# Optimization experiments

Hardware: AMD Instinct MI355X
Metric: run time of the kernel (lower is better)

## Reference

```python
import jax, jax.numpy as jnp
import numpy as np

N, G, P = 512, 11560, 2000
E_SG, E_GP, E_PP = 1000000, 200000, 50000
HID, HEADS, L = 192, 4, 2
C = HID // HEADS
NQ, OUT = 20, 128
EPS = 1e-5


def setup_inputs():
    key = jax.random.key(0)
    ks = iter(jax.random.split(key, 64))
    def rn(shape, s=0.05):
        return jax.random.normal(next(ks), shape, jnp.float32) * s
    def ri(n, hi):
        return jax.random.randint(next(ks), (n,), 0, hi)
    return dict(
        x_sample=rn((N, HID), 1.0), x_gene=rn((G, HID), 1.0), x_pathway=rn((P, HID), 1.0),
        e_sg_src=ri(E_SG, N), e_sg_dst=ri(E_SG, G),
        e_gp_src=ri(E_GP, G), e_gp_dst=ri(E_GP, P),
        e_pp_src=ri(E_PP, P), e_pp_dst=ri(E_PP, P),
        sage_Wl=rn((L, 2, HID, HID)), sage_bl=jnp.zeros((L, 2, HID)), sage_Wr=rn((L, 2, HID, HID)),
        gat_Wl=rn((L, 3, HID, HID)), gat_bl=jnp.zeros((L, 3, HID)),
        gat_Wr=rn((L, 3, HID, HID)), gat_br=jnp.zeros((L, 3, HID)),
        gat_att=rn((L, 3, HEADS, C), 0.1), gat_bias=jnp.zeros((L, 3, HID)),
        ln_g=jnp.ones((L, 3, HID)), ln_b=jnp.zeros((L, 3, HID)),
        pool_query=rn((NQ, HID), 1.0),
        pool_in_w=rn((3 * HID, HID)), pool_in_b=jnp.zeros((3 * HID,)),
        pool_out_w=rn((HID, HID)), pool_out_b=jnp.zeros((HID,)),
        ff_w1=rn((HID, HID)), ff_b1=jnp.zeros((HID,)),
        ff_w2=rn((HID, HID)), ff_b2=jnp.zeros((HID,)),
        pool_ln_g=jnp.ones((HID,)), pool_ln_b=jnp.zeros((HID,)),
        proj_w=rn((OUT, HID)), proj_b=jnp.zeros((OUT,)),
    )


def _ln(x, g, b):
    mu = x.mean(-1, keepdims=True)
    v = ((x - mu) ** 2).mean(-1, keepdims=True)
    return (x - mu) / jnp.sqrt(v + EPS) * g + b


def _sage(x_src, x_dst, src, dst, Wl, bl, Wr, n_dst):
    # PyG SAGEConv: lin_l(mean_aggr(x_src[neighbors])) + lin_r(x_dst)
    s = jax.ops.segment_sum(x_src[src], dst, num_segments=n_dst)
    cnt = jax.ops.segment_sum(jnp.ones((src.shape[0],), x_src.dtype), dst, num_segments=n_dst)
    mean = s / jnp.maximum(cnt, 1.0)[:, None]
    return mean @ Wl.T + bl + x_dst @ Wr.T


def _gatv2(x_src, x_dst, src, dst, Wl, bl, Wr, br, att, bias, n_dst):
    # transform nodes first (cheap), then gather per edge
    gl = (x_src @ Wl.T + bl).reshape(-1, HEADS, C)[src]   # [E,H,C]
    gr = (x_dst @ Wr.T + br).reshape(-1, HEADS, C)[dst]   # [E,H,C]
    e = jax.nn.leaky_relu(gl + gr, 0.2)
    score = jnp.einsum('ehc,hc->eh', e, att)              # [E,H]
    m = jax.ops.segment_max(score, dst, num_segments=n_dst)
    ex = jnp.exp(score - m[dst])
    den = jax.ops.segment_sum(ex, dst, num_segments=n_dst)
    alpha = ex / (den[dst] + 1e-16)
    out = jax.ops.segment_sum(alpha[:, :, None] * gl, dst, num_segments=n_dst)
    return out.reshape(n_dst, HID) + bias


def reference(x_sample, x_gene, x_pathway, e_sg_src, e_sg_dst, e_gp_src, e_gp_dst,
              e_pp_src, e_pp_dst, sage_Wl, sage_bl, sage_Wr, gat_Wl, gat_bl, gat_Wr,
              gat_br, gat_att, gat_bias, ln_g, ln_b, pool_query, pool_in_w, pool_in_b,
              pool_out_w, pool_out_b, ff_w1, ff_b1, ff_w2, ff_b2, pool_ln_g, pool_ln_b,
              proj_w, proj_b):
    xs, xg, xp = x_sample, x_gene, x_pathway
    for l in range(L):
        og = _sage(xs, xg, e_sg_src, e_sg_dst, sage_Wl[l, 0], sage_bl[l, 0], sage_Wr[l, 0], G)
        os_ = _sage(xg, xs, e_sg_dst, e_sg_src, sage_Wl[l, 1], sage_bl[l, 1], sage_Wr[l, 1], N)
        op = _gatv2(xg, xp, e_gp_src, e_gp_dst, gat_Wl[l, 0], gat_bl[l, 0], gat_Wr[l, 0],
                    gat_br[l, 0], gat_att[l, 0], gat_bias[l, 0], P)
        og = og + _gatv2(xp, xg, e_gp_dst, e_gp_src, gat_Wl[l, 1], gat_bl[l, 1], gat_Wr[l, 1],
                         gat_br[l, 1], gat_att[l, 1], gat_bias[l, 1], G)
        op = op + _gatv2(xp, xp, e_pp_src, e_pp_dst, gat_Wl[l, 2], gat_bl[l, 2], gat_Wr[l, 2],
                         gat_br[l, 2], gat_att[l, 2], gat_bias[l, 2], P)
        # residual + LayerNorm (dropout = identity in eval)
        xs = _ln(xs + os_, ln_g[l, 0], ln_b[l, 0])
        xg = _ln(xg + og, ln_g[l, 1], ln_b[l, 1])
        xp = _ln(xp + op, ln_g[l, 2], ln_b[l, 2])
    # MultiQueryPooling over sample nodes (batch=1 MultiheadAttention)
    Wq, Wk, Wv = jnp.split(pool_in_w, 3, axis=0)
    bq, bk, bv = jnp.split(pool_in_b, 3, axis=0)
    q = (pool_query @ Wq.T + bq).reshape(NQ, HEADS, C)
    k = (xs @ Wk.T + bk).reshape(N, HEADS, C)
    v = (xs @ Wv.T + bv).reshape(N, HEADS, C)
    attn = jax.nn.softmax(jnp.einsum('qhc,nhc->hqn', q, k) / (C ** 0.5), axis=-1)
    o = jnp.einsum('hqn,nhc->qhc', attn, v).reshape(NQ, HID) @ pool_out_w.T + pool_out_b
    pooled = o.mean(0)  # [HID]
    h = jax.nn.relu(pooled @ ff_w1.T + ff_b1) @ ff_w2.T + ff_b2
    h = _ln(h, pool_ln_g, pool_ln_b)
    return (h @ proj_w.T + proj_b)[None, :]  # [1, OUT]
```

## Files before the change

kernel.cpp:

```cpp
#include <hip/hip_runtime.h>

#define N_S 512
#define N_G 11560
#define N_P 2000
#define NE_SG 1000000
#define NE_GP 200000
#define NE_PP 50000
#define HID 192
#define HEADS 4
#define CDIM 48
#define NQd 20
#define OUTD 128
#define LDK 12288
#define SPLITK 16
#define CHUNKK 768

typedef __attribute__((ext_vector_type(8))) short short8;
typedef __attribute__((ext_vector_type(4))) float float4v;

__device__ __forceinline__ float bf2f(unsigned short u){
  union { unsigned int i; float f; } x; x.i = ((unsigned int)u) << 16; return x.f;
}
__device__ __forceinline__ unsigned short f2bf(float f){
  union { float f; unsigned int i; } u; u.f = f;
  unsigned int r = u.i + 0x7FFFu + ((u.i >> 16) & 1u);
  return (unsigned short)(r >> 16);
}
__device__ __forceinline__ ushort4 f4bf(float4 v){
  return make_ushort4(f2bf(v.x), f2bf(v.y), f2bf(v.z), f2bf(v.w));
}

__global__ __launch_bounds__(256) void k_detect(const unsigned int* __restrict__ raw,
                                                int* __restrict__ flag){
  __shared__ int cnt;
  if (threadIdx.x == 0) cnt = 0;
  __syncthreads();
  int c = 0;
  for (int i = threadIdx.x; i < 2048; i += 256) {
    float f = __uint_as_float(raw[i]);
    float a = fabsf(f);
    if (f == f && a > 1e-4f && a < 1000.0f) c++;
  }
  atomicAdd(&cnt, c);
  __syncthreads();
  if (threadIdx.x == 0) flag[0] = (cnt >= 1024) ? 1 : 0;
}

#define NLOAD 27
#define LOADBX 2048
struct LoadDesc { const void* src; float* dst; int n; };
struct LoadTable { LoadDesc d[NLOAD]; };
__global__ __launch_bounds__(256)
void k_load_all(LoadTable tab, const int* __restrict__ flag){
  LoadDesc de = tab.d[blockIdx.y];
  int fp32 = flag[0];
  for (int i = blockIdx.x*256 + threadIdx.x; i < de.n; i += LOADBX*256) {
    if (fp32) de.dst[i] = ((const float*)de.src)[i];
    else      de.dst[i] = bf2f(((const unsigned short*)de.src)[i]);
  }
}

__global__ __launch_bounds__(256)
void k_cntbuild(const int* __restrict__ src, const int* __restrict__ dst,
                int* __restrict__ cg, int E){
  int i = blockIdx.x*256 + threadIdx.x;
  if (i >= E) return;
  atomicAdd(&cg[(size_t)dst[i]*N_S + src[i]], 1);
}

__global__ __launch_bounds__(256)
void k_cvtT(const int* __restrict__ cg, unsigned short* __restrict__ bfA,
            unsigned short* __restrict__ bfB){
  __shared__ unsigned short tile[64][68];
  int g0 = blockIdx.x*64, s0 = blockIdx.y*64;
  int t = threadIdx.x; int r = t>>2, seg = t&3;
  int g = g0 + r;
  if (g < N_G) {
    const int* row = cg + (size_t)g*N_S + s0 + seg*16;
    unsigned short* arow = bfA + (size_t)g*N_S + s0 + seg*16;
    #pragma unroll
    for (int i=0;i<16;i++){
      unsigned short v = f2bf((float)row[i]);
      tile[r][seg*16+i] = v;
      arow[i] = v;
    }
  } else {
    #pragma unroll
    for (int i=0;i<16;i++) tile[r][seg*16+i] = 0;
  }
  __syncthreads();
  int s = s0 + r;
  unsigned short* brow = bfB + (size_t)s*LDK + g0 + seg*16;
  #pragma unroll
  for (int i=0;i<16;i++) brow[i] = tile[seg*16+i][r];
}

__global__ __launch_bounds__(256)
void k_rowinv_i(const int* __restrict__ A, int lda, int cols, int n,
                float* __restrict__ outp){
  int row = blockIdx.x*4 + (threadIdx.x >> 6);
  if (row >= n) return;
  int lane = threadIdx.x & 63;
  const int* Ar = A + (size_t)row*lda;
  float s = 0.0f;
  for (int c = lane; c < cols; c += 64) s += (float)Ar[c];
  #pragma unroll
  for (int o = 32; o; o >>= 1) s += __shfl_xor(s, o);
  if (lane == 0) outp[row] = 1.0f / fmaxf(s, 1.0f);
}
__global__ __launch_bounds__(256)
void k_rowinv_h(const unsigned short* __restrict__ A, int lda, int cols, int n,
                float* __restrict__ outp){
  int row = blockIdx.x*4 + (threadIdx.x >> 6);
  if (row >= n) return;
  int lane = threadIdx.x & 63;
  const unsigned short* Ar = A + (size_t)row*lda;
  float s = 0.0f;
  for (int c = lane; c < cols; c += 64) s += bf2f(Ar[c]);
  #pragma unroll
  for (int o = 32; o; o >>= 1) s += __shfl_xor(s, o);
  if (lane == 0) outp[row] = 1.0f / fmaxf(s, 1.0f);
}

__global__ __launch_bounds__(256)
void k_transpose(const float* __restrict__ in, unsigned short* __restrict__ outp,
                 int n, int ldo){
  __shared__ float tile[64][65];
  int r0 = blockIdx.x*64, c0 = blockIdx.y*64;
  int t = threadIdx.x;
  int r = t >> 2, seg = t & 3;
  int grr = r0 + r;
  if (grr < n) {
    #pragma unroll
    for (int i = 0; i < 4; i++) {
      float4 v = *(const float4*)(in + (size_t)grr*HID + c0 + seg*16 + i*4);
      tile[r][seg*16+i*4+0] = v.x; tile[r][seg*16+i*4+1] = v.y;
      tile[r][seg*16+i*4+2] = v.z; tile[r][seg*16+i*4+3] = v.w;
    }
  } else {
    #pragma unroll
    for (int i = 0; i < 16; i++) tile[r][seg*16+i] = 0.0f;
  }
  __syncthreads();
  int w = t >> 6, lane = t & 63;
  if (r0 + lane < ldo) {
    #pragma unroll
    for (int j = 0; j < 16; j++) {
      int c = w*16 + j;
      outp[(size_t)(c0+c)*ldo + r0 + lane] = f2bf(tile[lane][c]);
    }
  }
}

struct CsrJob { const int* src; const int* dst; int E; int n;
                int* deg; int* rowptr; int* cursor; int* col; };
struct CsrJobs { CsrJob j[3]; };

__global__ __launch_bounds__(256) void k_hist3(CsrJobs jobs){
  CsrJob jb = jobs.j[blockIdx.y];
  int i = blockIdx.x*256 + threadIdx.x;
  if (i < jb.E) atomicAdd(&jb.deg[jb.dst[i]], 1);
}
__global__ __launch_bounds__(256) void k_scan3(CsrJobs jobs){
  CsrJob jb = jobs.j[blockIdx.x];
  __shared__ int part[256];
  __shared__ int pre[256];
  int t = threadIdx.x;
  int n = jb.n;
  int C = (n + 255) >> 8;
  int lo = t*C, hi = min(n, lo + C);
  int s = 0;
  for (int i = lo; i < hi; i++) s += jb.deg[i];
  part[t] = s;
  __syncthreads();
  if (t == 0) {
    int acc = 0;
    for (int i = 0; i < 256; i++) { pre[i] = acc; acc += part[i]; }
    jb.rowptr[n] = acc;
  }
  __syncthreads();
  int run = pre[t];
  for (int i = lo; i < hi; i++) {
    jb.rowptr[i] = run; jb.cursor[i] = run; run += jb.deg[i];
  }
}
__global__ __launch_bounds__(256) void k_fill3(CsrJobs jobs){
  CsrJob jb = jobs.j[blockIdx.y];
  int i = blockIdx.x*256 + threadIdx.x;
  if (i >= jb.E) return;
  int pos = atomicAdd(&jb.cursor[jb.dst[i]], 1);
  jb.col[pos] = jb.src[i];
}

#define LDA 200
__global__ __launch_bounds__(256)
void k_gemm(const float* __restrict__ A, const float* __restrict__ rowscale,
            const float* __restrict__ W, const float* __restrict__ bias,
            float* __restrict__ outp, int n, int accum)
{
  __shared__ __align__(16) unsigned short Asm[64*LDA];
  __shared__ __align__(16) unsigned short Wsm[64*LDA];
  int t = threadIdx.x;
  int row0 = blockIdx.x * 64;
  int col0 = blockIdx.y * 64;
  {
    int r = t >> 2, seg = t & 3;
    int gr = row0 + r;
    unsigned short* ad = Asm + r*LDA + seg*48;
    if (gr < n) {
      float sc = rowscale ? rowscale[gr] : 1.0f;
      const float* Ar = A + (size_t)gr*HID + seg*48;
      #pragma unroll
      for (int i = 0; i < 12; i++) {
        float4 v = *reinterpret_cast<const float4*>(Ar + i*4);
        v.x *= sc; v.y *= sc; v.z *= sc; v.w *= sc;
        *reinterpret_cast<ushort4*>(ad + i*4) = f4bf(v);
      }
    } else {
      ushort4 z = make_ushort4(0,0,0,0);
      #pragma unroll
      for (int i = 0; i < 12; i++) *reinterpret_cast<ushort4*>(ad + i*4) = z;
    }
    const float* Wr = W + (size_t)(col0 + r)*HID + seg*48;
    unsigned short* wd = Wsm + r*LDA + seg*48;
    #pragma unroll
    for (int i = 0; i < 12; i++) {
      float4 v = *reinterpret_cast<const float4*>(Wr + i*4);
      *reinterpret_cast<ushort4*>(wd + i*4) = f4bf(v);
    }
  }
  __syncthreads();
  int w = t >> 6, lane = t & 63;
  int quad = lane >> 4, mr = lane & 15;
  float4v acc[4] = {};
  const unsigned short* Abase = Asm + (w*16 + mr)*LDA + quad*8;
  const unsigned short* Wbase = Wsm + mr*LDA + quad*8;
  #pragma unroll
  for (int k0 = 0; k0 < 6; k0++) {
    short8 a = *reinterpret_cast<const short8*>(Abase + k0*32);
    #pragma unroll
    for (int ct = 0; ct < 4; ct++) {
      short8 b = *reinterpret_cast<const short8*>(Wbase + ct*16*LDA + k0*32);
      acc[ct] = __builtin_amdgcn_mfma_f32_16x16x32_bf16(a, b, acc[ct], 0, 0, 0);
    }
  }
  #pragma unroll
  for (int ct = 0; ct < 4; ct++) {
    #pragma unroll
    for (int reg = 0; reg < 4; reg++) {
      int rr = row0 + w*16 + quad*4 + reg;
      if (rr < n) {
        int cc = col0 + ct*16 + mr;
        float v = acc[ct][reg];
        if (bias) v += bias[cc];
        if (accum) v += outp[(size_t)rr*HID + cc];
        outp[(size_t)rr*HID + cc] = v;
      }
    }
  }
}

struct GemmJob { const float* A; const float* W; const float* bias;
                 unsigned short* out; int n; };
struct GemmJobs { GemmJob j[6]; int rb[7]; };
__global__ __launch_bounds__(256)
void k_gemm6(GemmJobs jobs)
{
  int bx = blockIdx.x;
  int z = 0;
  #pragma unroll
  for (int q = 1; q < 6; q++) if (bx >= jobs.rb[q]) z = q;
  GemmJob jb = jobs.j[z];
  int row0 = (bx - jobs.rb[z]) * 64;
  __shared__ __align__(16) unsigned short Asm[64*LDA];
  __shared__ __align__(16) unsigned short Wsm[64*LDA];
  int t = threadIdx.x;
  int col0 = blockIdx.y * 64;
  {
    int r = t >> 2, seg = t & 3;
    int gr = row0 + r;
    unsigned short* ad = Asm + r*LDA + seg*48;
    if (gr < jb.n) {
      const float* Ar = jb.A + (size_t)gr*HID + seg*48;
      #pragma unroll
      for (int i = 0; i < 12; i++) {
        float4 v = *reinterpret_cast<const float4*>(Ar + i*4);
        *reinterpret_cast<ushort4*>(ad + i*4) = f4bf(v);
      }
    } else {
      ushort4 zz = make_ushort4(0,0,0,0);
      #pragma unroll
      for (int i = 0; i < 12; i++) *reinterpret_cast<ushort4*>(ad + i*4) = zz;
    }
    const float* Wr = jb.W + (size_t)(col0 + r)*HID + seg*48;
    unsigned short* wd = Wsm + r*LDA + seg*48;
    #pragma unroll
    for (int i = 0; i < 12; i++) {
      float4 v = *reinterpret_cast<const float4*>(Wr + i*4);
      *reinterpret_cast<ushort4*>(wd + i*4) = f4bf(v);
    }
  }
  __syncthreads();
  int w = t >> 6, lane = t & 63;
  int quad = lane >> 4, mr = lane & 15;
  float4v acc[4] = {};
  const unsigned short* Abase = Asm + (w*16 + mr)*LDA + quad*8;
  const unsigned short* Wbase = Wsm + mr*LDA + quad*8;
  #pragma unroll
  for (int k0 = 0; k0 < 6; k0++) {
    short8 a = *reinterpret_cast<const short8*>(Abase + k0*32);
    #pragma unroll
    for (int ct = 0; ct < 4; ct++) {
      short8 b = *reinterpret_cast<const short8*>(Wbase + ct*16*LDA + k0*32);
      acc[ct] = __builtin_amdgcn_mfma_f32_16x16x32_bf16(a, b, acc[ct], 0, 0, 0);
    }
  }
  #pragma unroll
  for (int ct = 0; ct < 4; ct++) {
    #pragma unroll
    for (int reg = 0; reg < 4; reg++) {
      int rr = row0 + w*16 + quad*4 + reg;
      if (rr < jb.n) {
        int cc = col0 + ct*16 + mr;
        jb.out[(size_t)rr*HID + cc] = f2bf(acc[ct][reg] + jb.bias[cc]);
      }
    }
  }
}

__global__ __launch_bounds__(256)
void k_gemm2(const float* __restrict__ A1, const float* __restrict__ rs1,
             const float* __restrict__ W1,
             const float* __restrict__ A2, const float* __restrict__ W2,
             const float* __restrict__ bias,
             float* __restrict__ outp, int n)
{
  __shared__ __align__(16) unsigned short Asm[64*LDA];
  __shared__ __align__(16) unsigned short Wsm[64*LDA];
  int t = threadIdx.x;
  int row0 = blockIdx.x * 64;
  int col0 = blockIdx.y * 64;
  int r = t >> 2, seg = t & 3;
  int w = t >> 6, lane = t & 63;
  int quad = lane >> 4, mr = lane & 15;
  float4v acc[4] = {};
  for (int p = 0; p < 2; p++) {
    if (p) __syncthreads();
    const float* A = p ? A2 : A1;
    const float* W = p ? W2 : W1;
    {
      int gr = row0 + r;
      unsigned short* ad = Asm + r*LDA + seg*48;
      if (gr < n) {
        float sc = (!p && rs1) ? rs1[gr] : 1.0f;
        const float* Ar = A + (size_t)gr*HID + seg*48;
        #pragma unroll
        for (int i = 0; i < 12; i++) {
          float4 v = *reinterpret_cast<const float4*>(Ar + i*4);
          v.x *= sc; v.y *= sc; v.z *= sc; v.w *= sc;
          *reinterpret_cast<ushort4*>(ad + i*4) = f4bf(v);
        }
      } else {
        ushort4 z = make_ushort4(0,0,0,0);
        #pragma unroll
        for (int i = 0; i < 12; i++) *reinterpret_cast<ushort4*>(ad + i*4) = z;
      }
      const float* Wr = W + (size_t)(col0 + r)*HID + seg*48;
      unsigned short* wd = Wsm + r*LDA + seg*48;
      #pragma unroll
      for (int i = 0; i < 12; i++) {
        float4 v = *reinterpret_cast<const float4*>(Wr + i*4);
        *reinterpret_cast<ushort4*>(wd + i*4) = f4bf(v);
      }
    }
    __syncthreads();
    const unsigned short* Abase = Asm + (w*16 + mr)*LDA + quad*8;
    const unsigned short* Wbase = Wsm + mr*LDA + quad*8;
    #pragma unroll
    for (int k0 = 0; k0 < 6; k0++) {
      short8 a = *reinterpret_cast<const short8*>(Abase + k0*32);
      #pragma unroll
      for (int ct = 0; ct < 4; ct++) {
        short8 b = *reinterpret_cast<const short8*>(Wbase + ct*16*LDA + k0*32);
        acc[ct] = __builtin_amdgcn_mfma_f32_16x16x32_bf16(a, b, acc[ct], 0, 0, 0);
      }
    }
  }
  #pragma unroll
  for (int ct = 0; ct < 4; ct++) {
    #pragma unroll
    for (int reg = 0; reg < 4; reg++) {
      int rr = row0 + w*16 + quad*4 + reg;
      if (rr < n) {
        int cc = col0 + ct*16 + mr;
        outp[(size_t)rr*HID + cc] = acc[ct][reg] + bias[cc];
      }
    }
  }
}

#define BKG 128
#define LDG 136
__global__ __launch_bounds__(256)
void k_gemm_g(const unsigned short* __restrict__ A, int lda,
              const unsigned short* __restrict__ W, int ldw,
              float* __restrict__ outp, int n, int K)
{
  __shared__ __align__(16) unsigned short Asm[64*LDG];
  __shared__ __align__(16) unsigned short Wsm[64*LDG];
  int t = threadIdx.x;
  int row0 = blockIdx.x * 64;
  int col0 = blockIdx.y * 64;
  int r = t >> 2, seg = t & 3;
  int w = t >> 6, lane = t & 63;
  int quad = lane >> 4, mr = lane & 15;
  float4v acc[4] = {};
  for (int k0 = 0; k0 < K; k0 += BKG) {
    {
      int gr = row0 + r;
      unsigned short* ad = Asm + r*LDG + seg*32;
      if (gr < n) {
        const unsigned short* Ar = A + (size_t)gr*lda + k0 + seg*32;
        #pragma unroll
        for (int i = 0; i < 4; i++) *(uint4*)(ad + i*8) = *(const uint4*)(Ar + i*8);
      } else {
        uint4 z = make_uint4(0,0,0,0);
        #pragma unroll
        for (int i = 0; i < 4; i++) *(uint4*)(ad + i*8) = z;
      }
      const unsigned short* Wr = W + (size_t)(col0 + r)*ldw + k0 + seg*32;
      unsigned short* wd = Wsm + r*LDG + seg*32;
      #pragma unroll
      for (int i = 0; i < 4; i++) *(uint4*)(wd + i*8) = *(const uint4*)(Wr + i*8);
    }
    __syncthreads();
    const unsigned short* Abase = Asm + (w*16 + mr)*LDG + quad*8;
    const unsigned short* Wbase = Wsm + mr*LDG + quad*8;
    #pragma unroll
    for (int kk = 0; kk < 4; kk++) {
      short8 a = *(const short8*)(Abase + kk*32);
      #pragma unroll
      for (int ct = 0; ct < 4; ct++) {
        short8 b = *(const short8*)(Wbase + ct*16*LDG + kk*32);
        acc[ct] = __builtin_amdgcn_mfma_f32_16x16x32_bf16(a, b, acc[ct], 0, 0, 0);
      }
    }
    __syncthreads();
  }
  #pragma unroll
  for (int ct = 0; ct < 4; ct++) {
    #pragma unroll
    for (int reg = 0; reg < 4; reg++) {
      int rr = row0 + w*16 + quad*4 + reg;
      if (rr < n) outp[(size_t)rr*HID + col0 + ct*16 + mr] = acc[ct][reg];
    }
  }
}

__global__ __launch_bounds__(256)
void k_gemm_sk(const unsigned short* __restrict__ A, int lda,
               const unsigned short* __restrict__ W, int ldw,
               float* __restrict__ part, int n)
{
  __shared__ __align__(16) unsigned short Asm[64*LDG];
  __shared__ __align__(16) unsigned short Wsm[64*LDG];
  int t = threadIdx.x;
  int row0 = blockIdx.x * 64;
  int col0 = blockIdx.y * 64;
  int kz   = blockIdx.z;
  int kbeg = kz * CHUNKK;
  int r = t >> 2, seg = t & 3;
  int w = t >> 6, lane = t & 63;
  int quad = lane >> 4, mr = lane & 15;
  float4v acc[4] = {};
  for (int k0 = kbeg; k0 < kbeg + CHUNKK; k0 += BKG) {
    {
      int gr = row0 + r;
      unsigned short* ad = Asm + r*LDG + seg*32;
      if (gr < n) {
        const unsigned short* Ar = A + (size_t)gr*lda + k0 + seg*32;
        #pragma unroll
        for (int i = 0; i < 4; i++) *(uint4*)(ad + i*8) = *(const uint4*)(Ar + i*8);
      } else {
        uint4 z = make_uint4(0,0,0,0);
        #pragma unroll
        for (int i = 0; i < 4; i++) *(uint4*)(ad + i*8) = z;
      }
      const unsigned short* Wr = W + (size_t)(col0 + r)*ldw + k0 + seg*32;
      unsigned short* wd = Wsm + r*LDG + seg*32;
      #pragma unroll
      for (int i = 0; i < 4; i++) *(uint4*)(wd + i*8) = *(const uint4*)(Wr + i*8);
    }
    __syncthreads();
    const unsigned short* Abase = Asm + (w*16 + mr)*LDG + quad*8;
    const unsigned short* Wbase = Wsm + mr*LDG + quad*8;
    #pragma unroll
    for (int kk = 0; kk < 4; kk++) {
      short8 a = *(const short8*)(Abase + kk*32);
      #pragma unroll
      for (int ct = 0; ct < 4; ct++) {
        short8 b = *(const short8*)(Wbase + ct*16*LDG + kk*32);
        acc[ct] = __builtin_amdgcn_mfma_f32_16x16x32_bf16(a, b, acc[ct], 0, 0, 0);
      }
    }
    __syncthreads();
  }
  float* pd = part + (size_t)kz*n*HID;
  #pragma unroll
  for (int ct = 0; ct < 4; ct++) {
    #pragma unroll
    for (int reg = 0; reg < 4; reg++) {
      int rr = row0 + w*16 + quad*4 + reg;
      if (rr < n) pd[(size_t)rr*HID + col0 + ct*16 + mr] = acc[ct][reg];
    }
  }
}

__global__ __launch_bounds__(256)
void k_reduce_sk(const float* __restrict__ part, float* __restrict__ outp, int n){
  int i = blockIdx.x*256 + threadIdx.x;
  if (i >= n*HID) return;
  float s = 0.0f;
  #pragma unroll
  for (int z = 0; z < SPLITK; z++) s += part[(size_t)z*n*HID + i];
  outp[i] = s;
}

struct GatJob { const unsigned short* gl; const unsigned short* gr;
                const int* rowptr; const int* col;
                const float* att; const float* bias; float* out; int ndst; int accum; };
struct GatJobs { GatJob j[3]; int bo[4]; };

__global__ __launch_bounds__(256)
void k_gat_all(GatJobs jobs)
{
  int bx = blockIdx.x;
  int jz = 0;
  if (bx >= jobs.bo[1]) jz = 1;
  if (bx >= jobs.bo[2]) jz = 2;
  GatJob jb = jobs.j[jz];
  int tid = threadIdx.x;
  int w = tid >> 6, lane = tid & 63;
  int dst = (bx - jobs.bo[jz])*4 + w;
  bool active = dst < jb.ndst;
  __shared__ float attS[HID];
  __shared__ float grS[4][HID];
  __shared__ float swS[4][4][16];
  __shared__ int   sidxS[4][16];
  __shared__ float fS[4][4];
  __shared__ float lS[4][4];
  if (tid < HID) attS[tid] = jb.att[tid];
  if (active) {
    const unsigned short* grr = jb.gr + (size_t)dst*HID;
    grS[w][lane]     = bf2f(grr[lane]);
    grS[w][lane+64]  = bf2f(grr[lane+64]);
    grS[w][lane+128] = bf2f(grr[lane+128]);
  }
  __syncthreads();
  if (!active) return;

  int h16 = lane >> 4, j16 = lane & 15;
  int start = jb.rowptr[dst], end = jb.rowptr[dst+1];
  float m = -1e30f, l = 0.0f;
  float acc0 = 0.f, acc1 = 0.f, acc2 = 0.f;
  int hd0 = lane/48, hd1 = (lane+64)/48, hd2 = (lane+128)/48;
  const float* attH = attS + h16*CDIM;
  const float* grH  = grS[w] + h16*CDIM;

  for (int c0 = start; c0 < end; c0 += 16) {
    int nc = min(16, end - c0);
    float sc = -1e30f; int s = -1;
    if (j16 < nc) {
      s = jb.col[c0 + j16];
      const unsigned short* glr = jb.gl + (size_t)s*HID + h16*CDIM;
      float a = 0.0f;
      #pragma unroll
      for (int c = 0; c < CDIM; c++) {
        float v = bf2f(glr[c]) + grH[c];
        v = v > 0.0f ? v : 0.2f*v;
        a += v * attH[c];
      }
      sc = a;
    }
    if (h16 == 0) sidxS[w][j16] = s;
    float cm = sc;
    cm = fmaxf(cm, __shfl_xor(cm, 1));
    cm = fmaxf(cm, __shfl_xor(cm, 2));
    cm = fmaxf(cm, __shfl_xor(cm, 4));
    cm = fmaxf(cm, __shfl_xor(cm, 8));
    float nm = fmaxf(m, cm);
    float f = __expf(m - nm);
    l *= f;
    float e = (j16 < nc) ? __expf(sc - nm) : 0.0f;
    swS[w][h16][j16] = e;
    float cl = e;
    cl += __shfl_xor(cl, 1);
    cl += __shfl_xor(cl, 2);
    cl += __shfl_xor(cl, 4);
    cl += __shfl_xor(cl, 8);
    l += cl;
    m = nm;
    if (j16 == 0) fS[w][h16] = f;
    acc0 *= fS[w][hd0]; acc1 *= fS[w][hd1]; acc2 *= fS[w][hd2];
    for (int j = 0; j < nc; j++) {
      const unsigned short* glr = jb.gl + (size_t)sidxS[w][j]*HID;
      acc0 += swS[w][hd0][j] * bf2f(glr[lane]);
      acc1 += swS[w][hd1][j] * bf2f(glr[lane+64]);
      acc2 += swS[w][hd2][j] * bf2f(glr[lane+128]);
    }
  }
  if (j16 == 0) lS[w][h16] = l;
  float* od = jb.out + (size_t)dst*HID;
  float v0 = acc0 / (lS[w][hd0] + 1e-16f) + jb.bias[lane];
  float v1 = acc1 / (lS[w][hd1] + 1e-16f) + jb.bias[lane+64];
  float v2 = acc2 / (lS[w][hd2] + 1e-16f) + jb.bias[lane+128];
  if (jb.accum) { v0 += od[lane]; v1 += od[lane+64]; v2 += od[lane+128]; }
  od[lane] = v0; od[lane+64] = v1; od[lane+128] = v2;
}

__global__ __launch_bounds__(64)
void k_ln3(float* __restrict__ xs, const float* __restrict__ osb,
           float* __restrict__ xg, const float* __restrict__ og,
           float* __restrict__ xp, const float* __restrict__ opb,
           const float* __restrict__ op2,
           const float* __restrict__ LNg, const float* __restrict__ LNb, int l)
{
  int r = blockIdx.x;
  float* x; const float* d1; const float* d2 = nullptr; int typ;
  if (r < N_S)            { x = xs + (size_t)r*HID; d1 = osb + (size_t)r*HID; typ = 0; }
  else if (r < N_S + N_G) { int rr = r - N_S; x = xg + (size_t)rr*HID; d1 = og + (size_t)rr*HID; typ = 1; }
  else                    { int rr = r - N_S - N_G; x = xp + (size_t)rr*HID; d1 = opb + (size_t)rr*HID;
                            d2 = op2 + (size_t)rr*HID; typ = 2; }
  const float* g = LNg + (l*3 + typ)*HID;
  const float* b = LNb + (l*3 + typ)*HID;
  int lane = threadIdx.x;
  float v[3]; float sum = 0.0f;
  #pragma unroll
  for (int j=0;j<3;j++){
    int d = j*64 + lane;
    float t = x[d] + d1[d];
    if (d2) t += d2[d];
    v[j] = t; sum += t;
  }
  #pragma unroll
  for (int o=32;o;o>>=1) sum += __shfl_xor(sum, o);
  float mu = sum * (1.0f/HID);
  float var = 0.0f;
  #pragma unroll
  for (int j=0;j<3;j++){ float dd = v[j]-mu; var += dd*dd; }
  #pragma unroll
  for (int o=32;o;o>>=1) var += __shfl_xor(var, o);
  var *= (1.0f/HID);
  float inv = rsqrtf(var + 1e-5f);
  #pragma unroll
  for (int j=0;j<3;j++){
    int d = j*64 + lane;
    x[d] = (v[j]-mu)*inv*g[d] + b[d];
  }
}

__global__ __launch_bounds__(256)
void k_pool_attn(const float* __restrict__ qb, const float* __restrict__ kb,
                 const float* __restrict__ vb, float* __restrict__ ob)
{
  int h = blockIdx.x & 3;
  int q = blockIdx.x >> 2;
  __shared__ float prob[N_S];
  __shared__ float red[256];
  int t = threadIdx.x;
  const float* qrow = qb + (size_t)q*HID + h*CDIM;
  const float scale = 0.14433756729740643f;
  for (int n = t; n < N_S; n += 256) {
    const float* krow = kb + (size_t)n*HID + h*CDIM;
    float s = 0.0f;
    #pragma unroll 8
    for (int c=0;c<CDIM;c++) s += qrow[c]*krow[c];
    prob[n] = s * scale;
  }
  __syncthreads();
  float m = -1e30f;
  for (int n=t;n<N_S;n+=256) m = fmaxf(m, prob[n]);
  red[t] = m; __syncthreads();
  for (int s2=128;s2;s2>>=1){ if (t<s2) red[t]=fmaxf(red[t],red[t+s2]); __syncthreads(); }
  m = red[0]; __syncthreads();
  float sum = 0.0f;
  for (int n=t;n<N_S;n+=256){ float e=__expf(prob[n]-m); prob[n]=e; sum+=e; }
  red[t] = sum; __syncthreads();
  for (int s2=128;s2;s2>>=1){ if (t<s2) red[t]+=red[t+s2]; __syncthreads(); }
  float inv = 1.0f/red[0];
  __syncthreads();
  if (t < CDIM) {
    float acc = 0.0f;
    for (int n=0;n<N_S;n++) acc += prob[n]*vb[(size_t)n*HID + h*CDIM + t];
    ob[(size_t)q*HID + h*CDIM + t] = acc * inv;
  }
}

__global__ __launch_bounds__(192)
void k_tail(const float* __restrict__ ob2,
            const float* ffw1, const float* ffb1,
            const float* ffw2, const float* ffb2,
            const float* lng, const float* lnb,
            const float* pw, const float* pb,
            void* __restrict__ outp, const int* __restrict__ flag)
{
  __shared__ float pooled[HID];
  __shared__ float hh[HID];
  __shared__ float stats[2];
  int t = threadIdx.x;
  float a = 0.0f;
  for (int q=0;q<NQd;q++) a += ob2[q*HID + t];
  pooled[t] = a * (1.0f/NQd);
  __syncthreads();
  float s1 = ffb1[t];
  for (int k=0;k<HID;k++) s1 += pooled[k]*ffw1[t*HID+k];
  hh[t] = fmaxf(s1, 0.0f);
  __syncthreads();
  float s2 = ffb2[t];
  for (int k=0;k<HID;k++) s2 += hh[k]*ffw2[t*HID+k];
  __syncthreads();
  hh[t] = s2;
  __syncthreads();
  if (t == 0) {
    float mu=0.0f; for (int k=0;k<HID;k++) mu += hh[k];
    mu *= (1.0f/HID);
    float v=0.0f; for (int k=0;k<HID;k++){ float d=hh[k]-mu; v+=d*d; }
    v *= (1.0f/HID);
    stats[0]=mu; stats[1]=rsqrtf(v + 1e-5f);
  }
  __syncthreads();
  pooled[t] = (hh[t]-stats[0])*stats[1]*lng[t] + lnb[t];
  __syncthreads();
  if (t < OUTD) {
    float acc = pb[t];
    for (int k=0;k<HID;k++) acc += pooled[k]*pw[t*HID+k];
    if (flag[0]) ((float*)outp)[t] = acc;
    else         ((unsigned short*)outp)[t] = f2bf(acc);
  }
}

extern "C" void kernel_launch(void* const* d_in, const int* in_sizes, int n_in,
                              void* d_out, int out_size, void* d_ws, size_t ws_size,
                              hipStream_t stream)
{
  const int* sg_src = (const int*)d_in[3];
  const int* sg_dst = (const int*)d_in[4];
  const int* gp_src = (const int*)d_in[5];
  const int* gp_dst = (const int*)d_in[6];
  const int* pp_src = (const int*)d_in[7];
  const int* pp_dst = (const int*)d_in[8];

  float* base = (float*)d_ws;
  size_t off = 0;
  auto alloc = [&](size_t nf){ nf = (nf + 3) & ~(size_t)3; float* p = base + off; off += nf; return p; };
  int*   flag = (int*)alloc(4);
  float* xs   = alloc((size_t)N_S*HID);
  float* xg   = alloc((size_t)N_G*HID);
  float* xp   = alloc((size_t)N_P*HID);
  float* qin  = alloc((size_t)NQd*HID);
  float* Wsl  = alloc(2*2*HID*HID); float* bsl = alloc(2*2*HID); float* Wsr = alloc(2*2*HID*HID);
  float* Wgl  = alloc(2*3*HID*HID); float* bgl = alloc(2*3*HID);
  float* Wgr  = alloc(2*3*HID*HID); float* bgr = alloc(2*3*HID);
  float* Agat = alloc(2*3*HEADS*CDIM); float* Bgat = alloc(2*3*HID);
  float* LNg  = alloc(2*3*HID); float* LNb = alloc(2*3*HID);
  float* Pinw = alloc(3*HID*HID); float* Pinb = alloc(3*HID);
  float* Poutw= alloc(HID*HID);   float* Poutb= alloc(HID);
  float* Fw1  = alloc(HID*HID);   float* Fb1  = alloc(HID);
  float* Fw2  = alloc(HID*HID);   float* Fb2  = alloc(HID);
  float* PLg  = alloc(HID);       float* PLb  = alloc(HID);
  float* Pw   = alloc(OUTD*HID);  float* Pb   = alloc(OUTD);
  float* agg  = alloc((size_t)N_G*HID);
  float* aggS = alloc((size_t)N_S*HID);
  float* og   = alloc((size_t)N_G*HID);
  float* osb  = alloc((size_t)N_S*HID);
  float* opb  = alloc((size_t)N_P*HID);
  float* op2  = alloc((size_t)N_P*HID);
  unsigned short* glGb  = (unsigned short*)alloc((size_t)N_G*HID/2);
  unsigned short* grGb  = (unsigned short*)alloc((size_t)N_G*HID/2);
  unsigned short* grP0b = (unsigned short*)alloc((size_t)N_P*HID/2);
  unsigned short* glP1b = (unsigned short*)alloc((size_t)N_P*HID/2);
  unsigned short* glP2b = (unsigned short*)alloc((size_t)N_P*HID/2);
  unsigned short* grP2b = (unsigned short*)alloc((size_t)N_P*HID/2);
  float* qbuf = alloc((size_t)NQd*HID);
  float* kbuf = alloc((size_t)N_S*HID);
  float* vbuf = alloc((size_t)N_S*HID);
  float* obuf = alloc((size_t)NQd*HID);
  float* ob2  = alloc((size_t)NQd*HID);
  int*            CntGi = (int*)alloc((size_t)N_G*N_S);
  unsigned short* CntGb = (unsigned short*)alloc((size_t)N_G*N_S/2);
  unsigned short* CntSb = (unsigned short*)alloc((size_t)N_S*LDK/2);
  unsigned short* xsTb  = (unsigned short*)alloc((size_t)HID*N_S/2);
  unsigned short* xgTb  = (unsigned short*)alloc((size_t)HID*LDK/2);
  float* part = alloc((size_t)SPLITK*N_S*HID);
  float* invdegG = alloc(N_G);
  float* invdegS = alloc(N_S);
  int* degAll = (int*)alloc(2*N_P + N_G + 4);
  int* curAll = (int*)alloc(2*N_P + N_G + 4);
  int* rp_gp_p = (int*)alloc(N_P+2);  int* col_gp_p = (int*)alloc(NE_GP);
  int* rp_gp_g = (int*)alloc(N_G+2);  int* col_gp_g = (int*)alloc(NE_GP);
  int* rp_pp_p = (int*)alloc(N_P+2);  int* col_pp_p = (int*)alloc(NE_PP);
  (void)ws_size; (void)in_sizes; (void)n_in; (void)out_size;

  k_detect<<<1,256,0,stream>>>((const unsigned int*)d_in[0], flag);

  {
    LoadTable tab;
    int k = 0;
    auto add = [&](int i, float* dst, int n){ tab.d[k].src = d_in[i]; tab.d[k].dst = dst; tab.d[k].n = n; k++; };
    add(0,  xs,  N_S*HID);  add(1,  xg,  N_G*HID);  add(2,  xp,  N_P*HID);
    add(9,  Wsl, 2*2*HID*HID); add(10, bsl, 2*2*HID); add(11, Wsr, 2*2*HID*HID);
    add(12, Wgl, 2*3*HID*HID); add(13, bgl, 2*3*HID);
    add(14, Wgr, 2*3*HID*HID); add(15, bgr, 2*3*HID);
    add(16, Agat, 2*3*HEADS*CDIM); add(17, Bgat, 2*3*HID);
    add(18, LNg, 2*3*HID); add(19, LNb, 2*3*HID);
    add(20, qin, NQd*HID);
    add(21, Pinw, 3*HID*HID); add(22, Pinb, 3*HID);
    add(23, Poutw, HID*HID);  add(24, Poutb, HID);
    add(25, Fw1, HID*HID); add(26, Fb1, HID);
    add(27, Fw2, HID*HID); add(28, Fb2, HID);
    add(29, PLg, HID); add(30, PLb, HID);
    add(31, Pw, OUTD*HID); add(32, Pb, OUTD);
    k_load_all<<<dim3(LOADBX, NLOAD),256,0,stream>>>(tab, flag);
  }

  hipMemsetAsync(CntGi, 0, (size_t)N_G*N_S*4, stream);
  hipMemsetAsync(degAll, 0, (size_t)(2*N_P + N_G)*4, stream);
  k_cntbuild<<<(NE_SG+255)/256,256,0,stream>>>(sg_src, sg_dst, CntGi, NE_SG);
  k_cvtT<<<dim3(LDK/64, N_S/64),256,0,stream>>>(CntGi, CntGb, CntSb);
  k_rowinv_i<<<(N_G+3)/4,256,0,stream>>>(CntGi, N_S, N_S, N_G, invdegG);
  k_rowinv_h<<<(N_S+3)/4,256,0,stream>>>(CntSb, LDK, LDK, N_S, invdegS);

  {
    CsrJobs jobs;
    jobs.j[0] = { gp_src, gp_dst, NE_GP, N_P, degAll,           rp_gp_p, curAll,           col_gp_p };
    jobs.j[1] = { gp_dst, gp_src, NE_GP, N_G, degAll+N_P,       rp_gp_g, curAll+N_P,       col_gp_g };
    jobs.j[2] = { pp_src, pp_dst, NE_PP, N_P, degAll+N_P+N_G,   rp_pp_p, curAll+N_P+N_G,   col_pp_p };
    k_hist3<<<dim3((NE_GP+255)/256, 3),256,0,stream>>>(jobs);
    k_scan3<<<3,256,0,stream>>>(jobs);
    k_fill3<<<dim3((NE_GP+255)/256, 3),256,0,stream>>>(jobs);
  }

  const int RB_G = (N_G+63)/64, RB_P = (N_P+63)/64;
  const int GB_P = (N_P+3)/4,  GB_G = (N_G+3)/4;

  for (int l=0; l<2; l++) {
    k_transpose<<<dim3(8,3),256,0,stream>>>(xs, xsTb, N_S, N_S);
    k_gemm_g<<<dim3(RB_G,3),256,0,stream>>>(CntGb, N_S, xsTb, N_S, agg, N_G, N_S);
    k_gemm2<<<dim3(RB_G,3),256,0,stream>>>(agg, invdegG,
        Wsl + (size_t)(l*2+0)*HID*HID, xg, Wsr + (size_t)(l*2+0)*HID*HID,
        bsl + (l*2+0)*HID, og, N_G);

    k_transpose<<<dim3(LDK/64,3),256,0,stream>>>(xg, xgTb, N_G, LDK);
    k_gemm_sk<<<dim3(8,3,SPLITK),256,0,stream>>>(CntSb, LDK, xgTb, LDK, part, N_S);
    k_reduce_sk<<<(N_S*HID+255)/256,256,0,stream>>>(part, aggS, N_S);
    k_gemm2<<<dim3((N_S+63)/64,3),256,0,stream>>>(aggS, invdegS,
        Wsl + (size_t)(l*2+1)*HID*HID, xs, Wsr + (size_t)(l*2+1)*HID*HID,
        bsl + (l*2+1)*HID, osb, N_S);

    {
      GemmJobs gj;
      int w0 = l*3+0, w1 = l*3+1, w2 = l*3+2;
      gj.j[0] = { xg, Wgl + (size_t)w0*HID*HID, bgl + w0*HID, glGb,  N_G };
      gj.j[1] = { xp, Wgr + (size_t)w0*HID*HID, bgr + w0*HID, grP0b, N_P };
      gj.j[2] = { xp, Wgl + (size_t)w1*HID*HID, bgl + w1*HID, glP1b, N_P };
      gj.j[3] = { xg, Wgr + (size_t)w1*HID*HID, bgr + w1*HID, grGb,  N_G };
      gj.j[4] = { xp, Wgl + (size_t)w2*HID*HID, bgl + w2*HID, glP2b, N_P };
      gj.j[5] = { xp, Wgr + (size_t)w2*HID*HID, bgr + w2*HID, grP2b, N_P };
      int nrb[6] = { RB_G, RB_P, RB_P, RB_G, RB_P, RB_P };
      gj.rb[0] = 0;
      for (int q = 0; q < 6; q++) gj.rb[q+1] = gj.rb[q] + nrb[q];
      k_gemm6<<<dim3(gj.rb[6],3),256,0,stream>>>(gj);
    }
    {
      GatJobs gt;
      int w0 = l*3+0, w1 = l*3+1, w2 = l*3+2;
      gt.j[0] = { glGb,  grP0b, rp_gp_p, col_gp_p, Agat + (size_t)w0*HID, Bgat + (size_t)w0*HID, opb, N_P, 0 };
      gt.j[1] = { glP1b, grGb,  rp_gp_g, col_gp_g, Agat + (size_t)w1*HID, Bgat + (size_t)w1*HID, og,  N_G, 1 };
      gt.j[2] = { glP2b, grP2b, rp_pp_p, col_pp_p, Agat + (size_t)w2*HID, Bgat + (size_t)w2*HID, op2, N_P, 0 };
      gt.bo[0] = 0; gt.bo[1] = GB_P; gt.bo[2] = GB_P + GB_G; gt.bo[3] = GB_P + GB_G + GB_P;
      k_gat_all<<<dim3(gt.bo[3]),256,0,stream>>>(gt);
    }
    k_ln3<<<N_S+N_G+N_P,64,0,stream>>>(xs, osb, xg, og, xp, opb, op2, LNg, LNb, l);
  }

  k_gemm<<<dim3(1,3),256,0,stream>>>(qin, nullptr, Pinw, Pinb, qbuf, NQd, 0);
  k_gemm<<<dim3((N_S+63)/64,3),256,0,stream>>>(xs, nullptr,
      Pinw + (size_t)HID*HID, Pinb + HID, kbuf, N_S, 0);
  k_gemm<<<dim3((N_S+63)/64,3),256,0,stream>>>(xs, nullptr,
      Pinw + (size_t)2*HID*HID, Pinb + 2*HID, vbuf, N_S, 0);
  k_pool_attn<<<NQd*HEADS,256,0,stream>>>(qbuf, kbuf, vbuf, obuf);
  k_gemm<<<dim3(1,3),256,0,stream>>>(obuf, nullptr, Poutw, Poutb, ob2, NQd, 0);
  k_tail<<<1,HID,0,stream>>>(ob2, Fw1, Fb1, Fw2, Fb2, PLg, PLb, Pw, Pb, d_out, flag);
}
```

Before: 751.9 us.

## Merge transpose and pooling QKV launches; keep GAT att/gr in registers

Folds the two per-layer transposes into one grouped launch and the three pooling input projections into one grouped GEMM launch, which cuts kernel launch count. The GAT kernel now holds the attention vector and destination features in registers instead of shared memory. It drops the block-wide barrier and uses 16-byte vector loads for gathered source rows, with a launch-bounds occupancy hint. The 96 float registers per thread this adds could raise register pressure or cause spills.

Result: slower. 775.8 us (+3.2%).

```diff
diff --git a/kernel.cpp b/kernel.cpp
--- a/kernel.cpp
+++ b/kernel.cpp
@@ -122,11 +122,16 @@
   if (lane == 0) outp[row] = 1.0f / fmaxf(s, 1.0f);
 }
 
-__global__ __launch_bounds__(256)
-void k_transpose(const float* __restrict__ in, unsigned short* __restrict__ outp,
-                 int n, int ldo){
+struct TransJobs { const float* inA; unsigned short* outA; int nA; int ldoA; int rbA;
+                   const float* inB; unsigned short* outB; int nB; int ldoB; };
+__global__ __launch_bounds__(256)
+void k_transpose2(TransJobs tj){
+  const float* in; unsigned short* outp; int n, ldo, r0;
+  int bx = blockIdx.x;
+  if (bx < tj.rbA) { in = tj.inA; outp = tj.outA; n = tj.nA; ldo = tj.ldoA; r0 = bx*64; }
+  else             { in = tj.inB; outp = tj.outB; n = tj.nB; ldo = tj.ldoB; r0 = (bx - tj.rbA)*64; }
   __shared__ float tile[64][65];
-  int r0 = blockIdx.x*64, c0 = blockIdx.y*64;
+  int c0 = blockIdx.y*64;
   int t = threadIdx.x;
   int r = t >> 2, seg = t & 3;
   int grr = r0 + r;
@@ -323,6 +328,74 @@
       if (rr < jb.n) {
         int cc = col0 + ct*16 + mr;
         jb.out[(size_t)rr*HID + cc] = f2bf(acc[ct][reg] + jb.bias[cc]);
+      }
+    }
+  }
+}
+
+struct PoolJob { const float* A; const float* W; const float* bias;
+                 float* out; int n; };
+struct PoolJobs { PoolJob j[3]; int rb[4]; };
+__global__ __launch_bounds__(256)
+void k_gemm3(PoolJobs jobs)
+{
+  int bx = blockIdx.x;
+  int z = 0;
+  if (bx >= jobs.rb[1]) z = 1;
+  if (bx >= jobs.rb[2]) z = 2;
+  PoolJob jb = jobs.j[z];
+  int row0 = (bx - jobs.rb[z]) * 64;
+  __shared__ __align__(16) unsigned short Asm[64*LDA];
+  __shared__ __align__(16) unsigned short Wsm[64*LDA];
+  int t = threadIdx.x;
+  int col0 = blockIdx.y * 64;
+  {
+    int r = t >> 2, seg = t & 3;
+    int gr = row0 + r;
+    unsigned short* ad = Asm + r*LDA + seg*48;
+    if (gr < jb.n) {
+      const float* Ar = jb.A + (size_t)gr*HID + seg*48;
+      #pragma unroll
+      for (int i = 0; i < 12; i++) {
+        float4 v = *reinterpret_cast<const float4*>(Ar + i*4);
+        *reinterpret_cast<ushort4*>(ad + i*4) = f4bf(v);
+      }
+    } else {
+      ushort4 zz = make_ushort4(0,0,0,0);
+      #pragma unroll
+      for (int i = 0; i < 12; i++) *reinterpret_cast<ushort4*>(ad + i*4) = zz;
+    }
+    const float* Wr = jb.W + (size_t)(col0 + r)*HID + seg*48;
+    unsigned short* wd = Wsm + r*LDA + seg*48;
+    #pragma unroll
+    for (int i = 0; i < 12; i++) {
+      float4 v = *reinterpret_cast<const float4*>(Wr + i*4);
+      *reinterpret_cast<ushort4*>(wd + i*4) = f4bf(v);
+    }
+  }
+  __syncthreads();
+  int w = t >> 6, lane = t & 63;
+  int quad = lane >> 4, mr = lane & 15;
+  float4v acc[4] = {};
+  const unsigned short* Abase = Asm + (w*16 + mr)*LDA + quad*8;
+  const unsigned short* Wbase = Wsm + mr*LDA + quad*8;
+  #pragma unroll
+  for (int k0 = 0; k0 < 6; k0++) {
+    short8 a = *reinterpret_cast<const short8*>(Abase + k0*32);
+    #pragma unroll
+    for (int ct = 0; ct < 4; ct++) {
+      short8 b = *reinterpret_cast<const short8*>(Wbase + ct*16*LDA + k0*32);
+      acc[ct] = __builtin_amdgcn_mfma_f32_16x16x32_bf16(a, b, acc[ct], 0, 0, 0);
+    }
+  }
+  #pragma unroll
+  for (int ct = 0; ct < 4; ct++) {
+    #pragma unroll
+    for (int reg = 0; reg < 4; reg++) {
+      int rr = row0 + w*16 + quad*4 + reg;
+      if (rr < jb.n) {
+        int cc = col0 + ct*16 + mr;
+        jb.out[(size_t)rr*HID + cc] = acc[ct][reg] + jb.bias[cc];
       }
     }
   }
@@ -531,7 +604,7 @@
                 const float* att; const float* bias; float* out; int ndst; int accum; };
 struct GatJobs { GatJob j[3]; int bo[4]; };
 
-__global__ __launch_bounds__(256)
+__global__ __launch_bounds__(256, 3)
 void k_gat_all(GatJobs jobs)
 {
   int bx = blockIdx.x;
@@ -542,43 +615,51 @@
   int tid = threadIdx.x;
   int w = tid >> 6, lane = tid & 63;
   int dst = (bx - jobs.bo[jz])*4 + w;
-  bool active = dst < jb.ndst;
-  __shared__ float attS[HID];
-  __shared__ float grS[4][HID];
+  if (dst >= jb.ndst) return;
   __shared__ float swS[4][4][16];
   __shared__ int   sidxS[4][16];
   __shared__ float fS[4][4];
   __shared__ float lS[4][4];
-  if (tid < HID) attS[tid] = jb.att[tid];
-  if (active) {
-    const unsigned short* grr = jb.gr + (size_t)dst*HID;
-    grS[w][lane]     = bf2f(grr[lane]);
-    grS[w][lane+64]  = bf2f(grr[lane+64]);
-    grS[w][lane+128] = bf2f(grr[lane+128]);
-  }
-  __syncthreads();
-  if (!active) return;
 
   int h16 = lane >> 4, j16 = lane & 15;
+  float attR[48], grR[48];
+  {
+    const float4* av = (const float4*)(jb.att + h16*CDIM);
+    #pragma unroll
+    for (int i = 0; i < 12; i++) {
+      float4 v = av[i];
+      attR[4*i+0] = v.x; attR[4*i+1] = v.y; attR[4*i+2] = v.z; attR[4*i+3] = v.w;
+    }
+    const short8* gv = (const short8*)(jb.gr + (size_t)dst*HID + h16*CDIM);
+    #pragma unroll
+    for (int i = 0; i < 6; i++) {
+      short8 g8 = gv[i];
+      #pragma unroll
+      for (int jj = 0; jj < 8; jj++) grR[8*i+jj] = bf2f((unsigned short)g8[jj]);
+    }
+  }
+
   int start = jb.rowptr[dst], end = jb.rowptr[dst+1];
   float m = -1e30f, l = 0.0f;
   float acc0 = 0.f, acc1 = 0.f, acc2 = 0.f;
   int hd0 = lane/48, hd1 = (lane+64)/48, hd2 = (lane+128)/48;
-  const float* attH = attS + h16*CDIM;
-  const float* grH  = grS[w] + h16*CDIM;
 
   for (int c0 = start; c0 < end; c0 += 16) {
     int nc = min(16, end - c0);
     float sc = -1e30f; int s = -1;
     if (j16 < nc) {
       s = jb.col[c0 + j16];
-      const unsigned short* glr = jb.gl + (size_t)s*HID + h16*CDIM;
+      const short8* glv = (const short8*)(jb.gl + (size_t)s*HID + h16*CDIM);
       float a = 0.0f;
       #pragma unroll
-      for (int c = 0; c < CDIM; c++) {
-        float v = bf2f(glr[c]) + grH[c];
-        v = v > 0.0f ? v : 0.2f*v;
-        a += v * attH[c];
+      for (int v8 = 0; v8 < 6; v8++) {
+        short8 g8 = glv[v8];
+        #pragma unroll
+        for (int jj = 0; jj < 8; jj++) {
+          float v = bf2f((unsigned short)g8[jj]) + grR[v8*8+jj];
+          v = v > 0.0f ? v : 0.2f*v;
+          a += v * attR[v8*8+jj];
+        }
       }
       sc = a;
     }
@@ -844,13 +925,17 @@
   const int GB_P = (N_P+3)/4,  GB_G = (N_G+3)/4;
 
   for (int l=0; l<2; l++) {
-    k_transpose<<<dim3(8,3),256,0,stream>>>(xs, xsTb, N_S, N_S);
+    {
+      TransJobs tj;
+      tj.inA = xs; tj.outA = xsTb; tj.nA = N_S; tj.ldoA = N_S; tj.rbA = 8;
+      tj.inB = xg; tj.outB = xgTb; tj.nB = N_G; tj.ldoB = LDK;
+      k_transpose2<<<dim3(8 + LDK/64, 3),256,0,stream>>>(tj);
+    }
     k_gemm_g<<<dim3(RB_G,3),256,0,stream>>>(CntGb, N_S, xsTb, N_S, agg, N_G, N_S);
     k_gemm2<<<dim3(RB_G,3),256,0,stream>>>(agg, invdegG,
         Wsl + (size_t)(l*2+0)*HID*HID, xg, Wsr + (size_t)(l*2+0)*HID*HID,
         bsl + (l*2+0)*HID, og, N_G);
 
-    k_transpose<<<dim3(LDK/64,3),256,0,stream>>>(xg, xgTb, N_G, LDK);
     k_gemm_sk<<<dim3(8,3,SPLITK),256,0,stream>>>(CntSb, LDK, xgTb, LDK, part, N_S);
     k_reduce_sk<<<(N_S*HID+255)/256,256,0,stream>>>(part, aggS, N_S);
     k_gemm2<<<dim3((N_S+63)/64,3),256,0,stream>>>(aggS, invdegS,
@@ -883,11 +968,14 @@
     k_ln3<<<N_S+N_G+N_P,64,0,stream>>>(xs, osb, xg, og, xp, opb, op2, LNg, LNb, l);
   }
 
-  k_gemm<<<dim3(1,3),256,0,stream>>>(qin, nullptr, Pinw, Pinb, qbuf, NQd, 0);
-  k_gemm<<<dim3((N_S+63)/64,3),256,0,stream>>>(xs, nullptr,
-      Pinw + (size_t)HID*HID, Pinb + HID, kbuf, N_S, 0);
-  k_gemm<<<dim3((N_S+63)/64,3),256,0,stream>>>(xs, nullptr,
-      Pinw + (size_t)2*HID*HID, Pinb + 2*HID, vbuf, N_S, 0);
+  {
+    PoolJobs pj;
+    pj.j[0] = { qin, Pinw,                     Pinb,         qbuf, NQd };
+    pj.j[1] = { xs,  Pinw + (size_t)HID*HID,   Pinb + HID,   kbuf, N_S };
+    pj.j[2] = { xs,  Pinw + (size_t)2*HID*HID, Pinb + 2*HID, vbuf, N_S };
+    pj.rb[0] = 0; pj.rb[1] = 1; pj.rb[2] = 1 + (N_S+63)/64; pj.rb[3] = pj.rb[2] + (N_S+63)/64;
+    k_gemm3<<<dim3(pj.rb[3],3),256,0,stream>>>(pj);
+  }
   k_pool_attn<<<NQd*HEADS,256,0,stream>>>(qbuf, kbuf, vbuf, obuf);
   k_gemm<<<dim3(1,3),256,0,stream>>>(obuf, nullptr, Poutw, Poutb, ob2, NQd, 0);
   k_tail<<<1,HID,0,stream>>>(ob2, Fw1, Fb1, Fw2, Fb2, PLg, PLb, Pw, Pb, d_out, flag);
```
